# Optimization experiments

Measured on AMD Instinct MI355X. Metric: run time of the kernel, lower is better.

## Reference

```python
import jax, jax.numpy as jnp
import numpy as np

HIDDEN = 1024
HEADS = 16
DK = HIDDEN // HEADS  # 64
B, N = 2, 2048


def setup_inputs() -> dict:
    key = jax.random.key(0)
    ks = jax.random.split(key, 12)
    s = 0.02
    return {
        "q": jax.random.normal(ks[0], (B, N, HIDDEN), jnp.float32),
        "k": jax.random.normal(ks[1], (B, N, HIDDEN), jnp.float32),
        "v": jax.random.normal(ks[2], (B, N, HIDDEN), jnp.float32),
        "attn_bias": jax.random.normal(ks[3], (B, N, N), jnp.float32),
        "attention_mask": jnp.zeros((B, N, N), jnp.float32),
        # projection weights stored [in, out]
        "Wq": jax.random.normal(ks[4], (HIDDEN, HIDDEN), jnp.float32) * s,
        "bq": jnp.zeros((HIDDEN,), jnp.float32),
        "Wk": jax.random.normal(ks[5], (HIDDEN, HIDDEN), jnp.float32) * s,
        "bk": jnp.zeros((HIDDEN,), jnp.float32),
        "Wv": jax.random.normal(ks[6], (HIDDEN, HIDDEN), jnp.float32) * s,
        "bv": jnp.zeros((HIDDEN,), jnp.float32),
        "Wo": jax.random.normal(ks[7], (HIDDEN, HIDDEN), jnp.float32) * s,
        "bo": jnp.zeros((HIDDEN,), jnp.float32),
    }


def reference(q, k, v, attn_bias, attention_mask, Wq, bq, Wk, bk, Wv, bv, Wo, bo):
    b, n, _ = q.shape
    scale = DK ** (-0.5)
    # project and split heads: [B, H, N, Dk]
    qh = (q @ Wq + bq).reshape(b, n, HEADS, DK).transpose(0, 2, 1, 3)
    kh = (k @ Wk + bk).reshape(b, -1, HEADS, DK).transpose(0, 2, 1, 3)
    vh = (v @ Wv + bv).reshape(b, -1, HEADS, DK).transpose(0, 2, 1, 3)
    # scaled scores + additive bias/mask broadcast over heads: [B, H, N, N]
    scores = jnp.einsum('bhnd,bhmd->bhnm', qh * scale, kh)
    scores = scores + attn_bias[:, None, :, :] + attention_mask[:, None, :, :]
    probs = jax.nn.softmax(scores, axis=-1)  # dropout is identity at inference
    ctx = jnp.einsum('bhnm,bhmd->bhnd', probs, vh)
    ctx = ctx.transpose(0, 2, 1, 3).reshape(b, n, HEADS * DK)
    return ctx @ Wo + bo
```

## Files before the change

### kernel.cpp

```cpp
#include <hip/hip_runtime.h>
#include <hip/hip_bf16.h>

#define HIDDEN 1024
#define NHEADS 16
#define DKH   64
#define BATCH 2
#define SEQ   2048
#define MTOT  (BATCH*SEQ)

using bf16x8 = __attribute__((ext_vector_type(8))) short;
using f32x4  = __attribute__((ext_vector_type(4))) float;
using u16x4  = __attribute__((ext_vector_type(4))) unsigned short;

__device__ __forceinline__ unsigned short f2bf(float f) {
    union { __hip_bfloat16 h; unsigned short u; } v;
    v.h = __float2bfloat16(f);
    return v.u;
}

__device__ __forceinline__ float asfloat(unsigned int u) {
    union { unsigned int u; float f; } v; v.u = u; return v.f;
}

__device__ __forceinline__ float fexp2(float x) {
#if __has_builtin(__builtin_amdgcn_exp2f)
    return __builtin_amdgcn_exp2f(x);
#else
    return exp2f(x);
#endif
}

__device__ __forceinline__ void gload16(const unsigned short* g, unsigned short* l) {
    __builtin_amdgcn_global_load_lds((const __attribute__((address_space(1))) void*)g,
                                     (__attribute__((address_space(3))) void*)l, 16, 0, 0);
}

#define L2E 1.44269504088896340736f

__global__ __launch_bounds__(256) void prep(const float4* __restrict__ q,
                                            const float4* __restrict__ k,
                                            const float4* __restrict__ v,
                                            u16x4* __restrict__ qkv_bf,
                                            const float* __restrict__ Wq,
                                            const float* __restrict__ Wk,
                                            const float* __restrict__ Wv,
                                            const float* __restrict__ Wo,
                                            unsigned short* __restrict__ wt,
                                            const float* __restrict__ bias,
                                            const float* __restrict__ mask,
                                            unsigned short* __restrict__ biasf) {
    __shared__ __align__(16) char sh[16640];
    float (*tile)[65] = (float (*)[65])sh;
    unsigned short (*lb)[520] = (unsigned short (*)[520])sh;
    const int bid = blockIdx.x, t = threadIdx.x;
    if (bid >= 2048) {
        const int r = bid - 2048;
        const int tensor = r >> 9;
        const float4* src = (tensor == 0) ? q : (tensor == 1) ? k : v;
        const int per = MTOT * HIDDEN / 4;
        const int base = (r & 511) * 2048 + t;
        float4 f[8];
        #pragma unroll
        for (int u = 0; u < 8; u++) f[u] = src[base + u * 256];
        u16x4* dst = qkv_bf + (size_t)tensor * per;
        #pragma unroll
        for (int u = 0; u < 8; u++) {
            u16x4 o;
            o.x = f2bf(f[u].x); o.y = f2bf(f[u].y); o.z = f2bf(f[u].z); o.w = f2bf(f[u].w);
            dst[base + u * 256] = o;
        }
    } else if (bid >= 1024) {
        int r = bid - 1024;
        const int z = r >> 8; r &= 255;
        const int kb = (r >> 4) * 64, nb = (r & 15) * 64;
        const float* W = (z == 0) ? Wq : (z == 1) ? Wk : (z == 2) ? Wv : Wo;
        unsigned short* out = wt + (size_t)z * HIDDEN * HIDDEN;
        #pragma unroll
        for (int i = 0; i < 16; i++) {
            int idx = i * 256 + t; int rr = idx >> 6, c = idx & 63;
            tile[rr][c] = W[(size_t)(kb + rr) * HIDDEN + nb + c];
        }
        __syncthreads();
        #pragma unroll
        for (int i = 0; i < 16; i++) {
            int idx = i * 256 + t; int n = idx >> 6, kk = idx & 63;
            out[(size_t)(nb + n) * HIDDEN + kb + kk] = f2bf(tile[kk][n]);
        }
    } else {
        const int cb = bid;
        const int chunk = cb & 3, g = (cb >> 2) & 127, b = cb >> 9;
        const float* bp = bias + ((size_t)b * SEQ + g * 16) * SEQ + chunk * 512;
        const float* mp = mask + ((size_t)b * SEQ + g * 16) * SEQ + chunk * 512;
        #pragma unroll
        for (int i = 0; i < 8; i++) {
            int idx = i * 256 + t;
            int row = idx >> 7, c4 = (idx & 127) * 4;
            float4 bv4 = *(const float4*)(bp + (size_t)row * SEQ + c4);
            float4 mv4 = *(const float4*)(mp + (size_t)row * SEQ + c4);
            union { u16x4 v; unsigned short s[4]; } o;
            o.s[0] = f2bf((bv4.x + mv4.x) * L2E);
            o.s[1] = f2bf((bv4.y + mv4.y) * L2E);
            o.s[2] = f2bf((bv4.z + mv4.z) * L2E);
            o.s[3] = f2bf((bv4.w + mv4.w) * L2E);
            *(u16x4*)&lb[row][c4] = o.v;
        }
        __syncthreads();
        const int w = t >> 6, ln = t & 63;
        const int quad = ln >> 4, c16 = ln & 15;
        unsigned short* ob = biasf + (((size_t)b * 128 + g) * 64 + chunk * 16) * 512 + ln * 8;
        #pragma unroll
        for (int it = 0; it < 4; it++) {
            int ttl = it * 4 + w;
            *(bf16x8*)(ob + (size_t)ttl * 512) = *(const bf16x8*)&lb[c16][ttl * 32 + quad * 8];
        }
    }
}

__device__ __forceinline__ void gemm_core_128(const unsigned short* __restrict__ X,
                                              const unsigned short* __restrict__ Wt,
                                              unsigned short* smem,
                                              int mbase, int nbase, f32x4 acc[4][4]) {
    const int tid = threadIdx.x, w = tid >> 6, ln = tid & 63;
    const int qr = (w >> 1) * 64, qc = (w & 1) * 64;
    const int g = ln >> 4, c16 = ln & 15;
    #pragma unroll
    for (int rt = 0; rt < 4; rt++)
        #pragma unroll
        for (int ct = 0; ct < 4; ct++) acc[rt][ct] = (f32x4){0.f, 0.f, 0.f, 0.f};

    for (int kk = 0; kk < HIDDEN; kk += 64) {
        __syncthreads();
        #pragma unroll
        for (int pass = 0; pass < 4; pass++) {
            int L = pass * 256 + tid;
            int r = L >> 3, c = (L & 7) ^ (r & 7);
            gload16(X  + (size_t)(mbase + r) * HIDDEN + kk + c * 8,
                    smem + (size_t)(pass * 256 + w * 64) * 8);
            gload16(Wt + (size_t)(nbase + r) * HIDDEN + kk + c * 8,
                    smem + 8192 + (size_t)(pass * 256 + w * 64) * 8);
        }
        __syncthreads();
        #pragma unroll
        for (int ks = 0; ks < 2; ks++) {
            bf16x8 af[4], bfr[4];
            #pragma unroll
            for (int rt = 0; rt < 4; rt++) {
                int r = qr + rt * 16 + c16;
                int ch = (g + ks * 4) ^ (r & 7);
                af[rt] = *(const bf16x8*)(smem + (size_t)(r * 8 + ch) * 8);
            }
            #pragma unroll
            for (int ct = 0; ct < 4; ct++) {
                int n = qc + ct * 16 + c16;
                int ch = (g + ks * 4) ^ (n & 7);
                bfr[ct] = *(const bf16x8*)(smem + 8192 + (size_t)(n * 8 + ch) * 8);
            }
            #pragma unroll
            for (int rt = 0; rt < 4; rt++)
                #pragma unroll
                for (int ct = 0; ct < 4; ct++)
                    acc[rt][ct] = __builtin_amdgcn_mfma_f32_16x16x32_bf16(af[rt], bfr[ct], acc[rt][ct], 0, 0, 0);
        }
    }
    __syncthreads();
}

__global__ __launch_bounds__(256, 2) void proj_gemm(const unsigned short* __restrict__ Xall,
                                                    const unsigned short* __restrict__ Wtall,
                                                    const float* __restrict__ bq,
                                                    const float* __restrict__ bk,
                                                    const float* __restrict__ bv,
                                                    unsigned short* __restrict__ qh,
                                                    unsigned short* __restrict__ khs,
                                                    unsigned short* __restrict__ vts) {
    __shared__ __align__(16) unsigned short smem[18432];
    const int z = blockIdx.z;
    const unsigned short* X  = Xall  + (size_t)z * MTOT * HIDDEN;
    const unsigned short* Wt = Wtall + (size_t)z * HIDDEN * HIDDEN;
    const float* bias = (z == 0) ? bq : (z == 1) ? bk : bv;
    const int mbase = blockIdx.x * 128, nbase = blockIdx.y * 128;
    const int tid = threadIdx.x, w = tid >> 6, ln = tid & 63;
    const int qr = (w >> 1) * 64, qc = (w & 1) * 64;
    const int g = ln >> 4, c16 = ln & 15;

    f32x4 acc[4][4];
    gemm_core_128(X, Wt, smem, mbase, nbase, acc);

    const float scale = (z == 0) ? (0.125f * L2E) : 1.0f;
    float bias_v[4];
    #pragma unroll
    for (int ct = 0; ct < 4; ct++) bias_v[ct] = bias[nbase + qc + ct * 16 + c16];

    unsigned short* eld = smem + w * 4608;
    #pragma unroll
    for (int rt = 0; rt < 4; rt++)
        #pragma unroll
        for (int ct = 0; ct < 4; ct++)
            #pragma unroll
            for (int r4 = 0; r4 < 4; r4++) {
                int row_l = rt * 16 + g * 4 + r4;
                int col_l = ct * 16 + c16;
                float val = (acc[rt][ct][r4] + bias_v[ct]) * scale;
                if (z == 2) eld[col_l * 72 + row_l] = f2bf(val);
                else        eld[row_l * 72 + col_l] = f2bf(val);
            }
    __syncthreads();

    const int b = mbase >> 11;
    const int pos0 = (mbase & 2047) + qr;
    const int h = (nbase + qc) >> 6;
    const int bh = b * NHEADS + h;
    if (z == 0) {
        const int row8 = ln >> 3, col8 = (ln & 7) * 8;
        unsigned short* dst0 = qh + ((size_t)bh * SEQ + pos0) * DKH;
        #pragma unroll
        for (int j = 0; j < 8; j++) {
            int row = j * 8 + row8;
            *(bf16x8*)(dst0 + row * 64 + col8) = *(const bf16x8*)&eld[row * 72 + col8];
        }
    } else if (z == 1) {
        unsigned short* base = khs + ((size_t)bh * 64 + (pos0 >> 5)) * 2048;
        const int kvp = (c16 >> 2) * 8 + (c16 & 3);
        #pragma unroll
        for (int j = 0; j < 8; j++) {
            int tloc = j >> 2, ks = (j >> 1) & 1, kvs = j & 1;
            int kvl = tloc * 32 + kvp + kvs * 4;
            *(bf16x8*)(base + tloc * 2048 + ks * 1024 + kvs * 512 + ln * 8)
                = *(const bf16x8*)&eld[kvl * 72 + ks * 32 + g * 8];
        }
    } else {
        unsigned short* base = vts + ((size_t)bh * 64 + (pos0 >> 5)) * 2048;
        #pragma unroll
        for (int j = 0; j < 8; j++) {
            int tloc = j >> 2, dt = j & 3;
            *(bf16x8*)(base + tloc * 2048 + dt * 512 + ln * 8)
                = *(const bf16x8*)&eld[(dt * 16 + c16) * 72 + tloc * 32 + g * 8];
        }
    }
}

__global__ __launch_bounds__(256, 4) void attn(const unsigned short* __restrict__ qh,
                                               const unsigned short* __restrict__ khs,
                                               const unsigned short* __restrict__ vts,
                                               const unsigned short* __restrict__ biasf,
                                               unsigned short* __restrict__ ctx) {
    __shared__ __align__(16) unsigned short smem[16384];
    const int tid = threadIdx.x, w = tid >> 6, ln = tid & 63;
    const int quad = ln >> 4, c16 = ln & 15;
    const int bid = blockIdx.x;
    const int xcd = bid & 7, jj = bid >> 3;
    const int bh = xcd * 4 + (jj >> 5);
    const int qb = jj & 31;
    const int b = bh >> 4, h = bh & 15;

    bf16x8 qf[2];
    {
        const unsigned short* qp = qh + ((size_t)bh * SEQ + qb * 64 + w * 16 + c16) * DKH + quad * 8;
        qf[0] = *(const bf16x8*)qp;
        qf[1] = *(const bf16x8*)(qp + 32);
    }

    const unsigned short* kT = khs + (size_t)bh * 131072;
    const unsigned short* vT = vts + (size_t)bh * 131072;
    const unsigned short* bb = biasf + (((size_t)b * 128 + qb * 4 + w) * 64) * 512 + ln * 8;

    f32x4 accv[4];
    #pragma unroll
    for (int dt = 0; dt < 4; dt++) accv[dt] = (f32x4){0.f, 0.f, 0.f, 0.f};
    float lacc = 0.f;

    bf16x8 bcur[4];
    #pragma unroll
    for (int j = 0; j < 4; j++) bcur[j] = *(const bf16x8*)(bb + j * 512);

    for (int T = 0; T < 16; T++) {
        __syncthreads();
        {
            const unsigned short* ksrc = kT + T * 8192 + w * 512 + ln * 8;
            const unsigned short* vsrc = vT + T * 8192 + w * 512 + ln * 8;
            unsigned short* lk = smem + w * 512;
            unsigned short* lv = smem + 8192 + w * 512;
            #pragma unroll
            for (int p = 0; p < 4; p++) {
                gload16(ksrc + p * 2048, lk + p * 2048);
                gload16(vsrc + p * 2048, lv + p * 2048);
            }
        }
        bf16x8 bnext[4];
        {
            const int Tn = (T < 15) ? T + 1 : 15;
            #pragma unroll
            for (int j = 0; j < 4; j++)
                bnext[j] = *(const bf16x8*)(bb + (Tn * 4 + j) * 512);
        }
        __syncthreads();
        #pragma unroll
        for (int j = 0; j < 4; j++) {
            bf16x8 kf00 = *(const bf16x8*)(smem + j * 2048 + ln * 8);
            bf16x8 kf01 = *(const bf16x8*)(smem + j * 2048 + 512 + ln * 8);
            bf16x8 kf10 = *(const bf16x8*)(smem + j * 2048 + 1024 + ln * 8);
            bf16x8 kf11 = *(const bf16x8*)(smem + j * 2048 + 1536 + ln * 8);
            bf16x8 vf[4];
            #pragma unroll
            for (int dt = 0; dt < 4; dt++)
                vf[dt] = *(const bf16x8*)(smem + 8192 + j * 2048 + dt * 512 + ln * 8);
            const unsigned int* bd = (const unsigned int*)&bcur[j];
            f32x4 s0, s1;
            s0[0] = asfloat(bd[0] << 16); s0[1] = asfloat(bd[0] & 0xFFFF0000u);
            s0[2] = asfloat(bd[1] << 16); s0[3] = asfloat(bd[1] & 0xFFFF0000u);
            s1[0] = asfloat(bd[2] << 16); s1[1] = asfloat(bd[2] & 0xFFFF0000u);
            s1[2] = asfloat(bd[3] << 16); s1[3] = asfloat(bd[3] & 0xFFFF0000u);
            s0 = __builtin_amdgcn_mfma_f32_16x16x32_bf16(kf00, qf[0], s0, 0, 0, 0);
            s0 = __builtin_amdgcn_mfma_f32_16x16x32_bf16(kf10, qf[1], s0, 0, 0, 0);
            s1 = __builtin_amdgcn_mfma_f32_16x16x32_bf16(kf01, qf[0], s1, 0, 0, 0);
            s1 = __builtin_amdgcn_mfma_f32_16x16x32_bf16(kf11, qf[1], s1, 0, 0, 0);
            #pragma unroll
            for (int r = 0; r < 4; r++) { s0[r] = fexp2(s0[r]); s1[r] = fexp2(s1[r]); }
            lacc += ((s0[0] + s0[1]) + (s0[2] + s0[3]))
                  + ((s1[0] + s1[1]) + (s1[2] + s1[3]));
            union { bf16x8 v; __hip_bfloat162 hh[4]; } pu;
            pu.hh[0] = __float22bfloat162_rn(make_float2(s0[0], s0[1]));
            pu.hh[1] = __float22bfloat162_rn(make_float2(s0[2], s0[3]));
            pu.hh[2] = __float22bfloat162_rn(make_float2(s1[0], s1[1]));
            pu.hh[3] = __float22bfloat162_rn(make_float2(s1[2], s1[3]));
            #pragma unroll
            for (int dt = 0; dt < 4; dt++)
                accv[dt] = __builtin_amdgcn_mfma_f32_16x16x32_bf16(vf[dt], pu.v, accv[dt], 0, 0, 0);
            bcur[j] = bnext[j];
        }
    }

    float l = lacc;
    l += __shfl_xor(l, 16);
    l += __shfl_xor(l, 32);
    const float inv = 1.0f / l;
    __syncthreads();
    unsigned short* ot = smem + w * 1152;
    #pragma unroll
    for (int dt = 0; dt < 4; dt++)
        #pragma unroll
        for (int r = 0; r < 4; r += 2) {
            union { __hip_bfloat162 hh; unsigned int u; } pk;
            pk.hh = __float22bfloat162_rn(make_float2(accv[dt][r] * inv,
                                                     accv[dt][r + 1] * inv));
            *(unsigned int*)&ot[c16 * 72 + dt * 16 + quad * 4 + r] = pk.u;
        }
    const int row = ln >> 2, seg = ln & 3;
    const unsigned short* srcp = ot + row * 72 + seg * 16;
    unsigned short* dstp = ctx + ((size_t)b * SEQ + qb * 64 + w * 16 + row) * HIDDEN
                         + h * 64 + seg * 16;
    *(bf16x8*)(dstp)     = *(const bf16x8*)(srcp);
    *(bf16x8*)(dstp + 8) = *(const bf16x8*)(srcp + 8);
}

__global__ __launch_bounds__(256, 2) void outproj(const unsigned short* __restrict__ X,
                                                  const unsigned short* __restrict__ Wt,
                                                  const float* __restrict__ bo,
                                                  float* __restrict__ out) {
    __shared__ __align__(16) unsigned short smem[16384];
    const int mbase = blockIdx.x * 128, nbase = blockIdx.y * 128;
    const int tid = threadIdx.x, w = tid >> 6, ln = tid & 63;
    const int qr = (w >> 1) * 64, qc = (w & 1) * 64;
    const int g = ln >> 4, c16 = ln & 15;

    f32x4 acc[4][4];
    gemm_core_128(X, Wt, smem, mbase, nbase, acc);

    float bo_v[4];
    #pragma unroll
    for (int ct = 0; ct < 4; ct++) bo_v[ct] = bo[nbase + qc + ct * 16 + c16];
    #pragma unroll
    for (int rt = 0; rt < 4; rt++)
        #pragma unroll
        for (int ct = 0; ct < 4; ct++)
            #pragma unroll
            for (int r4 = 0; r4 < 4; r4++)
                out[(size_t)(mbase + qr + rt * 16 + g * 4 + r4) * HIDDEN + nbase + qc + ct * 16 + c16]
                    = acc[rt][ct][r4] + bo_v[ct];
}

extern "C" void kernel_launch(void* const* d_in, const int* in_sizes, int n_in,
                              void* d_out, int out_size, void* d_ws, size_t ws_size,
                              hipStream_t stream) {
    const float* q    = (const float*)d_in[0];
    const float* k    = (const float*)d_in[1];
    const float* v    = (const float*)d_in[2];
    const float* bias = (const float*)d_in[3];
    const float* mask = (const float*)d_in[4];
    const float* Wq   = (const float*)d_in[5];
    const float* bq   = (const float*)d_in[6];
    const float* Wk   = (const float*)d_in[7];
    const float* bk   = (const float*)d_in[8];
    const float* Wv   = (const float*)d_in[9];
    const float* bv   = (const float*)d_in[10];
    const float* Wo   = (const float*)d_in[11];
    const float* bo   = (const float*)d_in[12];

    char* ws = (char*)d_ws;
    unsigned short* qkv_bf = (unsigned short*)(ws);
    unsigned short* wt     = (unsigned short*)(ws + 25165824);
    unsigned short* qh     = (unsigned short*)(ws + 33554432);
    unsigned short* khs    = (unsigned short*)(ws + 41943040);
    unsigned short* vts    = (unsigned short*)(ws + 50331648);
    unsigned short* ctx    = (unsigned short*)(ws + 58720256);
    unsigned short* biasf  = (unsigned short*)(ws + 67108864);

    prep<<<3584, 256, 0, stream>>>((const float4*)q, (const float4*)k, (const float4*)v,
                                   (u16x4*)qkv_bf, Wq, Wk, Wv, Wo, wt, bias, mask, biasf);
    proj_gemm<<<dim3(32, 8, 3), 256, 0, stream>>>(qkv_bf, wt, bq, bk, bv, qh, khs, vts);
    attn<<<1024, 256, 0, stream>>>(qh, khs, vts, biasf, ctx);
    outproj<<<dim3(32, 8), 256, 0, stream>>>(ctx, wt + (size_t)3 * HIDDEN * HIDDEN, bo,
                                             (float*)d_out);
}
```

Before: 280.6 us.

## Fuse fp32-to-bf16 activation conversion into projection GEMM tile loads

Removes the separate prep pass that converted q, k, v from fp32 to bf16 into a workspace buffer. The projection GEMM now loads fp32 activations straight into registers, converts them to bf16 and writes them swizzled into LDS, while weights still use direct global-to-LDS loads. This drops a full read-and-write round trip of 24 MB of activations. In exchange each GEMM tile reads twice the activation bytes (fp32), repeated across the 8 column blocks, and loses the async LDS-load path for the A operand.

```diff
diff --git a/kernel.cpp b/kernel.cpp
--- a/kernel.cpp
+++ b/kernel.cpp
@@ -37,11 +37,7 @@
 
 #define L2E 1.44269504088896340736f
 
-__global__ __launch_bounds__(256) void prep(const float4* __restrict__ q,
-                                            const float4* __restrict__ k,
-                                            const float4* __restrict__ v,
-                                            u16x4* __restrict__ qkv_bf,
-                                            const float* __restrict__ Wq,
+__global__ __launch_bounds__(256) void prep(const float* __restrict__ Wq,
                                             const float* __restrict__ Wk,
                                             const float* __restrict__ Wv,
                                             const float* __restrict__ Wo,
@@ -53,23 +49,7 @@
     float (*tile)[65] = (float (*)[65])sh;
     unsigned short (*lb)[520] = (unsigned short (*)[520])sh;
     const int bid = blockIdx.x, t = threadIdx.x;
-    if (bid >= 2048) {
-        const int r = bid - 2048;
-        const int tensor = r >> 9;
-        const float4* src = (tensor == 0) ? q : (tensor == 1) ? k : v;
-        const int per = MTOT * HIDDEN / 4;
-        const int base = (r & 511) * 2048 + t;
-        float4 f[8];
-        #pragma unroll
-        for (int u = 0; u < 8; u++) f[u] = src[base + u * 256];
-        u16x4* dst = qkv_bf + (size_t)tensor * per;
-        #pragma unroll
-        for (int u = 0; u < 8; u++) {
-            u16x4 o;
-            o.x = f2bf(f[u].x); o.y = f2bf(f[u].y); o.z = f2bf(f[u].z); o.w = f2bf(f[u].w);
-            dst[base + u * 256] = o;
-        }
-    } else if (bid >= 1024) {
+    if (bid >= 1024) {
         int r = bid - 1024;
         const int z = r >> 8; r &= 255;
         const int kb = (r >> 4) * 64, nb = (r & 15) * 64;
@@ -116,10 +96,11 @@
     }
 }
 
-__device__ __forceinline__ void gemm_core_128(const unsigned short* __restrict__ X,
-                                              const unsigned short* __restrict__ Wt,
-                                              unsigned short* smem,
-                                              int mbase, int nbase, f32x4 acc[4][4]) {
+template <bool AF32>
+__device__ __forceinline__ void gemm_core_128_t(const void* __restrict__ Xv,
+                                                const unsigned short* __restrict__ Wt,
+                                                unsigned short* smem,
+                                                int mbase, int nbase, f32x4 acc[4][4]) {
     const int tid = threadIdx.x, w = tid >> 6, ln = tid & 63;
     const int qr = (w >> 1) * 64, qc = (w & 1) * 64;
     const int g = ln >> 4, c16 = ln & 15;
@@ -130,14 +111,47 @@
 
     for (int kk = 0; kk < HIDDEN; kk += 64) {
         __syncthreads();
-        #pragma unroll
-        for (int pass = 0; pass < 4; pass++) {
-            int L = pass * 256 + tid;
-            int r = L >> 3, c = (L & 7) ^ (r & 7);
-            gload16(X  + (size_t)(mbase + r) * HIDDEN + kk + c * 8,
-                    smem + (size_t)(pass * 256 + w * 64) * 8);
-            gload16(Wt + (size_t)(nbase + r) * HIDDEN + kk + c * 8,
-                    smem + 8192 + (size_t)(pass * 256 + w * 64) * 8);
+        if constexpr (AF32) {
+            const float* Xf = (const float*)Xv;
+            float4 fa[4][2];
+            #pragma unroll
+            for (int pass = 0; pass < 4; pass++) {
+                int L = pass * 256 + tid;
+                int r = L >> 3, cc = L & 7;
+                const float* p = Xf + (size_t)(mbase + r) * HIDDEN + kk + cc * 8;
+                fa[pass][0] = *(const float4*)p;
+                fa[pass][1] = *(const float4*)(p + 4);
+            }
+            #pragma unroll
+            for (int pass = 0; pass < 4; pass++) {
+                int L = pass * 256 + tid;
+                int r = L >> 3, c = (L & 7) ^ (r & 7);
+                gload16(Wt + (size_t)(nbase + r) * HIDDEN + kk + c * 8,
+                        smem + 8192 + (size_t)(pass * 256 + w * 64) * 8);
+            }
+            #pragma unroll
+            for (int pass = 0; pass < 4; pass++) {
+                int L = pass * 256 + tid;
+                int r = L >> 3, cc = L & 7;
+                int cs = cc ^ (r & 7);
+                union { bf16x8 v; unsigned short s[8]; } o;
+                o.s[0] = f2bf(fa[pass][0].x); o.s[1] = f2bf(fa[pass][0].y);
+                o.s[2] = f2bf(fa[pass][0].z); o.s[3] = f2bf(fa[pass][0].w);
+                o.s[4] = f2bf(fa[pass][1].x); o.s[5] = f2bf(fa[pass][1].y);
+                o.s[6] = f2bf(fa[pass][1].z); o.s[7] = f2bf(fa[pass][1].w);
+                *(bf16x8*)(smem + (size_t)(r * 8 + cs) * 8) = o.v;
+            }
+        } else {
+            const unsigned short* X = (const unsigned short*)Xv;
+            #pragma unroll
+            for (int pass = 0; pass < 4; pass++) {
+                int L = pass * 256 + tid;
+                int r = L >> 3, c = (L & 7) ^ (r & 7);
+                gload16(X  + (size_t)(mbase + r) * HIDDEN + kk + c * 8,
+                        smem + (size_t)(pass * 256 + w * 64) * 8);
+                gload16(Wt + (size_t)(nbase + r) * HIDDEN + kk + c * 8,
+                        smem + 8192 + (size_t)(pass * 256 + w * 64) * 8);
+            }
         }
         __syncthreads();
         #pragma unroll
@@ -165,7 +179,9 @@
     __syncthreads();
 }
 
-__global__ __launch_bounds__(256, 2) void proj_gemm(const unsigned short* __restrict__ Xall,
+__global__ __launch_bounds__(256, 2) void proj_gemm(const float* __restrict__ qf32,
+                                                    const float* __restrict__ kf32,
+                                                    const float* __restrict__ vf32,
                                                     const unsigned short* __restrict__ Wtall,
                                                     const float* __restrict__ bq,
                                                     const float* __restrict__ bk,
@@ -175,7 +191,7 @@
                                                     unsigned short* __restrict__ vts) {
     __shared__ __align__(16) unsigned short smem[18432];
     const int z = blockIdx.z;
-    const unsigned short* X  = Xall  + (size_t)z * MTOT * HIDDEN;
+    const float* X  = (z == 0) ? qf32 : (z == 1) ? kf32 : vf32;
     const unsigned short* Wt = Wtall + (size_t)z * HIDDEN * HIDDEN;
     const float* bias = (z == 0) ? bq : (z == 1) ? bk : bv;
     const int mbase = blockIdx.x * 128, nbase = blockIdx.y * 128;
@@ -184,7 +200,7 @@
     const int g = ln >> 4, c16 = ln & 15;
 
     f32x4 acc[4][4];
-    gemm_core_128(X, Wt, smem, mbase, nbase, acc);
+    gemm_core_128_t<true>(X, Wt, smem, mbase, nbase, acc);
 
     const float scale = (z == 0) ? (0.125f * L2E) : 1.0f;
     float bias_v[4];
@@ -364,7 +380,7 @@
     const int g = ln >> 4, c16 = ln & 15;
 
     f32x4 acc[4][4];
-    gemm_core_128(X, Wt, smem, mbase, nbase, acc);
+    gemm_core_128_t<false>(X, Wt, smem, mbase, nbase, acc);
 
     float bo_v[4];
     #pragma unroll
@@ -397,7 +413,6 @@
     const float* bo   = (const float*)d_in[12];
 
     char* ws = (char*)d_ws;
-    unsigned short* qkv_bf = (unsigned short*)(ws);
     unsigned short* wt     = (unsigned short*)(ws + 25165824);
     unsigned short* qh     = (unsigned short*)(ws + 33554432);
     unsigned short* khs    = (unsigned short*)(ws + 41943040);
@@ -405,9 +420,8 @@
     unsigned short* ctx    = (unsigned short*)(ws + 58720256);
     unsigned short* biasf  = (unsigned short*)(ws + 67108864);
 
-    prep<<<3584, 256, 0, stream>>>((const float4*)q, (const float4*)k, (const float4*)v,
-                                   (u16x4*)qkv_bf, Wq, Wk, Wv, Wo, wt, bias, mask, biasf);
-    proj_gemm<<<dim3(32, 8, 3), 256, 0, stream>>>(qkv_bf, wt, bq, bk, bv, qh, khs, vts);
+    prep<<<2048, 256, 0, stream>>>(Wq, Wk, Wv, Wo, wt, bias, mask, biasf);
+    proj_gemm<<<dim3(32, 8, 3), 256, 0, stream>>>(q, k, v, wt, bq, bk, bv, qh, khs, vts);
     attn<<<1024, 256, 0, stream>>>(qh, khs, vts, biasf, ctx);
     outproj<<<dim3(32, 8), 256, 0, stream>>>(ctx, wt + (size_t)3 * HIDDEN * HIDDEN, bo,
                                              (float*)d_out);
```

After: 292.7 us. 1.04x slower.
